# Performance work log

Hardware: AMD Instinct MI355X
Metric: run time of the kernel (lower is better)

## Reference

```python
import jax, jax.numpy as jnp
import numpy as np

N = 20000          # num proposals (nodes)
E = 320000         # num edges
IN = 4096          # roi feature dim
EMB = 200          # glove embed dim
HID = 512          # hidden dim
NH = 8             # heads (conv1)
HC = HID // NH     # 64 per-head channels
NCLS = 151         # VG object classes
NEG_SLOPE = 0.2    # PyG GATConv leaky_relu slope


def setup_inputs() -> dict:
    key = jax.random.key(0)
    ks = jax.random.split(key, 18)
    d_in1 = IN + EMB + 128  # 4424, conv1 input dim
    inp = {
        "roi_features": jax.random.normal(ks[0], (N, IN), jnp.float32),
        "box_info": jax.random.uniform(ks[1], (N, 9), jnp.float32),
        # embedding tables
        "emb1": jax.random.normal(ks[2], (NCLS, EMB), jnp.float32) * 0.02,
        "emb2": jax.random.normal(ks[3], (NCLS, EMB), jnp.float32) * 0.02,
        # bbox MLP 9 -> 32 -> 128
        "bw1": jax.random.normal(ks[4], (9, 32), jnp.float32) / np.sqrt(9),
        "bb1": jnp.zeros((32,), jnp.float32),
        "bw2": jax.random.normal(ks[5], (32, 128), jnp.float32) / np.sqrt(32),
        "bb2": jnp.zeros((128,), jnp.float32),
        # GATConv1: d_in1 -> 8 heads x 64, concat
        "W1": jax.random.normal(ks[6], (d_in1, NH * HC), jnp.float32) / np.sqrt(d_in1),
        "a_src1": jax.random.normal(ks[7], (NH, HC), jnp.float32) * 0.1,
        "a_dst1": jax.random.normal(ks[8], (NH, HC), jnp.float32) * 0.1,
        "bias1": jnp.zeros((NH * HC,), jnp.float32),
        # GATConv2: 512 -> 512, 1 head, concat=False
        "W2": jax.random.normal(ks[9], (HID, HID), jnp.float32) / np.sqrt(HID),
        "a_src2": jax.random.normal(ks[10], (1, HID), jnp.float32) * 0.1,
        "a_dst2": jax.random.normal(ks[11], (1, HID), jnp.float32) * 0.1,
        "bias2": jnp.zeros((HID,), jnp.float32),
        # int inputs
        "obj_labels": jax.random.randint(ks[12], (N,), 0, NCLS, jnp.int32),
        "edge_index": jax.random.randint(ks[13], (2, E), 0, N, jnp.int32),
    }
    return inp


def _segment_softmax(logits, seg, n):
    # logits: [E, H]; softmax over edges sharing the same destination seg id
    m = jax.ops.segment_max(logits, seg, num_segments=n)
    e = jnp.exp(logits - m[seg])
    s = jax.ops.segment_sum(e, seg, num_segments=n)
    return e / (s[seg] + 1e-16)


def _gat_conv(x, src, dst, W, a_src, a_dst, bias, concat):
    # PyG GATConv (self-loops already included in src/dst); dropout off (eval)
    n = x.shape[0]
    H, C = a_src.shape
    h = (x @ W).reshape(n, H, C)                      # [N, H, C]
    al_s = jnp.einsum('nhc,hc->nh', h, a_src)         # [N, H]
    al_d = jnp.einsum('nhc,hc->nh', h, a_dst)
    logits = jax.nn.leaky_relu(al_s[src] + al_d[dst], NEG_SLOPE)  # [E, H]
    alpha = _segment_softmax(logits, dst, n)          # [E, H]
    out = jax.ops.segment_sum(alpha[:, :, None] * h[src], dst, num_segments=n)
    out = out.reshape(n, H * C) if concat else out.mean(axis=1)
    return out + bias


def reference(roi_features, box_info, emb1, emb2, bw1, bb1, bw2, bb2,
              W1, a_src1, a_dst1, bias1, W2, a_src2, a_dst2, bias2,
              obj_labels, edge_index):
    n = roi_features.shape[0]
    # predcls mode: GT labels -> embedding lookup
    obj_embed = emb1[obj_labels]                              # [N, 200]
    pos = jax.nn.relu(box_info @ bw1 + bb1)
    pos = jax.nn.relu(pos @ bw2 + bb2)                        # [N, 128]
    x = jnp.concatenate([roi_features, obj_embed, pos], -1)  # [N, 4424]

    # add self-loops (PyG GATConv default)
    ar = jnp.arange(n, dtype=edge_index.dtype)
    src = jnp.concatenate([edge_index[0], ar])
    dst = jnp.concatenate([edge_index[1], ar])

    edge_f1 = jax.nn.elu(_gat_conv(x, src, dst, W1, a_src1, a_dst1, bias1, True))
    obj_feats = _gat_conv(edge_f1, src, dst, W2, a_src2, a_dst2, bias2, False)

    obj_dists = jax.nn.one_hot(obj_labels, NCLS, dtype=jnp.float32)
    edge_pre_rep = jnp.concatenate([roi_features, obj_feats, emb2[obj_labels]], -1)
    return obj_dists, obj_labels, edge_pre_rep
```

## Files before the change

### kernel.cpp

```cpp
#include <hip/hip_runtime.h>
#include <hip/hip_bf16.h>

#define NNODES 20000
#define NEDGES 320000
#define ETOT   (NEDGES + NNODES)
#define KPADX  4224
#define SK     4
#define KC     (KPADX / SK)
#define MPAD   20096
#define NCLS   151
#define EPRW   4808
#define OUT_LAB_OFF  3020000L
#define OUT_EPR_OFF  3040000L
#define NSLOPE 0.2f

typedef __attribute__((ext_vector_type(8))) short bf16x8;
typedef __attribute__((ext_vector_type(4))) float f32x4;
typedef __attribute__((ext_vector_type(4))) short s16x4;

__device__ __forceinline__ short f2bf(float v) {
  union { __hip_bfloat16 b; short s; } u;
  u.b = __float2bfloat16(v);
  return u.s;
}

__device__ __forceinline__ float bf2f(short s) {
  union { float f; unsigned u; } x;
  x.u = ((unsigned)(unsigned short)s) << 16;
  return x.f;
}

__device__ __forceinline__ void gld16(const short* g, short* l) {
  __builtin_amdgcn_global_load_lds(
      (const __attribute__((address_space(1))) unsigned int*)g,
      (__attribute__((address_space(3))) unsigned int*)l, 16, 0, 0);
}

#define QB0 10000
#define QB1 (QB0 + 5000)
#define QB2 (QB1 + 1584)
#define QB3 (QB2 + 2112)
#define QB4 (QB3 + 256)
#define QB5 (QB4 + 1329)
#define QB6 (QB5 + 151)

__global__ __launch_bounds__(256) void mega_prep_kernel(
    const float* __restrict__ roi, const float* __restrict__ box,
    const float* __restrict__ emb1, const float* __restrict__ emb2,
    const float* __restrict__ bw1, const float* __restrict__ bb1,
    const float* __restrict__ bw2, const float* __restrict__ bb2,
    const float* __restrict__ W1, const float* __restrict__ W2,
    const int* __restrict__ labels, const int* __restrict__ ei,
    short* __restrict__ x, short* __restrict__ w1t, short* __restrict__ w2t,
    short* __restrict__ ef1, int* __restrict__ deg,
    float* __restrict__ als2, float* __restrict__ ald2,
    float* __restrict__ E1, float* __restrict__ dout) {
  const int b = blockIdx.x;
  const int tid = threadIdx.x;

  __shared__ float hids[4][32];
  __shared__ float tile[32][33];

  if (b < QB0) {
    const int base = b * 2048 + tid;
    f32x4 v[8];
#pragma unroll
    for (int k = 0; k < 8; ++k)
      v[k] = *(const f32x4*)&roi[(long)(base + k * 256) * 4];
#pragma unroll
    for (int k = 0; k < 8; ++k) {
      const int t = base + k * 256;
      const int node = t >> 10, cq = t & 1023;
      __builtin_nontemporal_store(v[k],
          (f32x4*)&dout[OUT_EPR_OFF + (long)node * EPRW + cq * 4]);
      s16x4 bb;
      bb.x = f2bf(v[k].x); bb.y = f2bf(v[k].y);
      bb.z = f2bf(v[k].z); bb.w = f2bf(v[k].w);
      *(s16x4*)&x[(long)node * KPADX + cq * 4] = bb;
    }
  } else if (b < QB1) {
    const int w = tid >> 6;
    const int lane = tid & 63;
    const int nd = (b - QB0) * 4 + w;
    if (lane < 32) {
      float a = bb1[lane];
#pragma unroll
      for (int i = 0; i < 9; ++i) a += box[nd * 9 + i] * bw1[i * 32 + lane];
      hids[w][lane] = a > 0.f ? a : 0.f;
    }
    __syncthreads();
    const long xrow = (long)nd * KPADX;
#pragma unroll
    for (int jj = 0; jj < 2; ++jj) {
      const int j = lane + jj * 64;
      float a = bb2[j];
#pragma unroll
      for (int i = 0; i < 32; ++i) a += hids[w][i] * bw2[i * 128 + j];
      a = a > 0.f ? a : 0.f;
      x[xrow + 4096 + j] = f2bf(a);
    }
    const int lab = labels[nd];
    float* epr = dout + OUT_EPR_OFF + (long)nd * EPRW;
    if (lane < 50) {
      const f32x4 e2 = *(const f32x4*)&emb2[lab * 200 + lane * 4];
      __builtin_nontemporal_store(e2, (f32x4*)&epr[4608 + lane * 4]);
    }
    for (int j = lane; j < NCLS; j += 64)
      dout[(long)nd * NCLS + j] = (j == lab) ? 1.f : 0.f;
    if (lane == 0) dout[OUT_LAB_OFF + nd] = (float)lab;
  } else if (b < QB2) {
    const int t = (b - QB1) * 256 + tid;
    if (t < 96 * KPADX) x[(long)NNODES * KPADX + t] = 0;
    if (t < 96 * 512)   ef1[(long)NNODES * 512 + t] = 0;
    if (t < MPAD)       { als2[t] = 0.f; ald2[t] = 0.f; }
  } else if (b < QB3) {
    const int t = b - QB2;
    const int n0 = (t % 16) * 32;
    const int k0 = (t / 16) * 32;
    const int tx = tid & 31, ty = tid >> 5;
#pragma unroll
    for (int i = ty; i < 32; i += 8) {
      const int kp = k0 + i;
      const int src = kp < 4096 ? kp : kp + 200;
      tile[i][tx] = W1[(long)src * 512 + (n0 + tx)];
    }
    __syncthreads();
#pragma unroll
    for (int i = ty; i < 32; i += 8)
      w1t[(long)(n0 + i) * KPADX + (k0 + tx)] = f2bf(tile[tx][i]);
  } else if (b < QB4) {
    const int t = b - QB3;
    const int n0 = (t % 16) * 32;
    const int k0 = (t / 16) * 32;
    const int tx = tid & 31, ty = tid >> 5;
#pragma unroll
    for (int i = ty; i < 32; i += 8)
      tile[i][tx] = W2[(long)(k0 + i) * 512 + (n0 + tx)];
    __syncthreads();
#pragma unroll
    for (int i = ty; i < 32; i += 8)
      w2t[(long)(n0 + i) * 512 + (k0 + tx)] = f2bf(tile[tx][i]);
  } else if (b < QB5) {
    const int e = (b - QB4) * 256 + tid;
    if (e < ETOT) {
      const int d = (e < NEDGES) ? ei[NEDGES + e] : (e - NEDGES);
      atomicAdd(&deg[d], 1);
    }
  } else {
    const int c = b - QB5;
#pragma unroll
    for (int jj = 0; jj < 2; ++jj) {
      const int j = tid + jj * 256;
      float a = 0.f;
      for (int k = 0; k < 200; ++k)
        a += emb1[c * 200 + k] * W1[(long)(4096 + k) * 512 + j];
      E1[c * 512 + j] = a;
    }
  }
}

__global__ __launch_bounds__(256) void scan_kernel(const int* __restrict__ deg,
                                                   int* __restrict__ off,
                                                   int* __restrict__ cur) {
  __shared__ int part[256];
  const int tid = threadIdx.x;
  const int chunk = (NNODES + 255) / 256;
  int start = tid * chunk;
  int end = start + chunk; if (end > NNODES) end = NNODES;
  int s = 0;
  for (int i = start; i < end; ++i) s += deg[i];
  part[tid] = s;
  __syncthreads();
  for (int d = 1; d < 256; d <<= 1) {
    const int v = (tid >= d) ? part[tid - d] : 0;
    __syncthreads();
    part[tid] += v;
    __syncthreads();
  }
  int base = part[tid] - s;
  for (int i = start; i < end; ++i) { off[i] = base; cur[i] = base; base += deg[i]; }
}

__global__ void csr_fill_kernel(const int* __restrict__ ei, int* __restrict__ cur,
                                int* __restrict__ csrs) {
  const int e = blockIdx.x * 256 + threadIdx.x;
  if (e >= ETOT) return;
  const int s = (e < NEDGES) ? ei[e] : (e - NEDGES);
  const int d = (e < NEDGES) ? ei[NEDGES + e] : (e - NEDGES);
  unsigned slot = (unsigned)atomicAdd(&cur[d], 1);
  if (slot >= ETOT) slot = 0;
  csrs[slot] = s;
}

__global__ __launch_bounds__(256) void gemm_split(const short* __restrict__ A,
                                                  const short* __restrict__ BT,
                                                  short* __restrict__ hp) {
  __shared__ short As[4096];
  __shared__ short Bs[4096];
  const int tid = threadIdx.x;
  const int lane = tid & 63;
  const int w = tid >> 6;
  const int wr = w >> 1, wc = w & 1;
  const int wid = (blockIdx.x & 7) * 314 + ((int)blockIdx.x >> 3);
  const long bm = (long)(wid >> 4) * 128;
  const int  sk = (wid >> 2) & 3;
  const long bn = (long)(wid & 3) * 128;

  f32x4 acc[4][4] = {};

  const short* gA0 = A + (bm + w * 32 + (lane >> 2)) * (long)KPADX + sk * KC + (lane & 3) * 8;
  const short* gA1 = gA0 + 16L * KPADX;
  const short* gB0 = BT + (bn + w * 32 + (lane >> 2)) * (long)KPADX + sk * KC + (lane & 3) * 8;
  const short* gB1 = gB0 + 16L * KPADX;
  short* lA0 = &As[w * 1024];
  short* lA1 = &As[w * 1024 + 512];
  short* lB0 = &Bs[w * 1024];
  short* lB1 = &Bs[w * 1024 + 512];

  const int ar = (wr * 64 + (lane & 15)) * 32 + (lane >> 4) * 8;
  const int br = (wc * 64 + (lane & 15)) * 32 + (lane >> 4) * 8;

  for (int k0 = 0; k0 < KC; k0 += 32) {
    gld16(gA0, lA0); gld16(gA1, lA1);
    gld16(gB0, lB0); gld16(gB1, lB1);
    gA0 += 32; gA1 += 32; gB0 += 32; gB1 += 32;
    asm volatile("s_waitcnt vmcnt(0)" ::: "memory");
    __syncthreads();
    bf16x8 a[4], b[4];
#pragma unroll
    for (int mi = 0; mi < 4; ++mi) a[mi] = *(const bf16x8*)&As[ar + mi * 512];
#pragma unroll
    for (int ni = 0; ni < 4; ++ni) b[ni] = *(const bf16x8*)&Bs[br + ni * 512];
#pragma unroll
    for (int mi = 0; mi < 4; ++mi)
#pragma unroll
      for (int ni = 0; ni < 4; ++ni)
        acc[mi][ni] = __builtin_amdgcn_mfma_f32_16x16x32_bf16(a[mi], b[ni], acc[mi][ni], 0, 0, 0);
    __syncthreads();
  }

  short* Cp = hp + (long)sk * MPAD * 512;
#pragma unroll
  for (int mi = 0; mi < 4; ++mi) {
#pragma unroll
    for (int ni = 0; ni < 4; ++ni) {
      const long row0 = bm + wr * 64 + mi * 16 + (lane >> 4) * 4;
      const long col  = bn + wc * 64 + ni * 16 + (lane & 15);
#pragma unroll
      for (int r = 0; r < 4; ++r)
        Cp[(row0 + r) * 512 + col] = f2bf(acc[mi][ni][r]);
    }
  }
}

__global__ __launch_bounds__(256) void reduce1_kernel(short* __restrict__ hp,
    const float* __restrict__ E1, const int* __restrict__ labels,
    const float* __restrict__ aS, const float* __restrict__ aD,
    float* __restrict__ als, float* __restrict__ ald) {
  const int row = blockIdx.x * 4 + (threadIdx.x >> 6);
  const int lane = threadIdx.x & 63;
  const int c0 = lane * 8;
  const long base = (long)row * 512 + c0;
  float v[8] = {};
#pragma unroll
  for (int s = 0; s < SK; ++s) {
    const bf16x8 p = *(const bf16x8*)&hp[(long)s * MPAD * 512 + base];
#pragma unroll
    for (int j = 0; j < 8; ++j) v[j] += bf2f(p[j]);
  }
  const int lab = (row < NNODES) ? labels[row] : 0;
  const float* e1r = E1 + (long)lab * 512;
#pragma unroll
  for (int j = 0; j < 8; ++j) v[j] += e1r[c0 + j];
  bf16x8 o;
#pragma unroll
  for (int j = 0; j < 8; ++j) o[j] = f2bf(v[j]);
  *(bf16x8*)&hp[base] = o;
  float s_ = 0.f, d_ = 0.f;
#pragma unroll
  for (int j = 0; j < 8; ++j) {
    s_ += v[j] * aS[c0 + j];
    d_ += v[j] * aD[c0 + j];
  }
#pragma unroll
  for (int oo = 1; oo < 8; oo <<= 1) {
    s_ += __shfl_xor(s_, oo);
    d_ += __shfl_xor(d_, oo);
  }
  if ((lane & 7) == 0) {
    const int head = lane >> 3;
    als[row * 8 + head] = s_;
    ald[row * 8 + head] = d_;
  }
}

__global__ __launch_bounds__(256) void gemm_bt(const short* __restrict__ A,
                                               const short* __restrict__ BT,
                                               short* __restrict__ C,
                                               const float* __restrict__ aS,
                                               const float* __restrict__ aD,
                                               float* __restrict__ als,
                                               float* __restrict__ ald,
                                               int Kpad, int Ncols, int H) {
  __shared__ short As[4096];
  __shared__ short Bs[4096];
  const int tid = threadIdx.x;
  const int lane = tid & 63;
  const int w = tid >> 6;
  const int wr = w >> 1, wc = w & 1;
  const int nbn = Ncols >> 7;
  const long bm = (long)((int)blockIdx.x / nbn) * 128;
  const long bn = (long)((int)blockIdx.x % nbn) * 128;

  f32x4 acc[4][4] = {};

  const short* gA0 = A + (bm + w * 32 + (lane >> 2)) * (long)Kpad + (lane & 3) * 8;
  const short* gA1 = gA0 + 16L * Kpad;
  const short* gB0 = BT + (bn + w * 32 + (lane >> 2)) * (long)Kpad + (lane & 3) * 8;
  const short* gB1 = gB0 + 16L * Kpad;
  short* lA0 = &As[w * 1024];
  short* lA1 = &As[w * 1024 + 512];
  short* lB0 = &Bs[w * 1024];
  short* lB1 = &Bs[w * 1024 + 512];

  const int ar = (wr * 64 + (lane & 15)) * 32 + (lane >> 4) * 8;
  const int br = (wc * 64 + (lane & 15)) * 32 + (lane >> 4) * 8;

  for (int k0 = 0; k0 < Kpad; k0 += 32) {
    gld16(gA0, lA0); gld16(gA1, lA1);
    gld16(gB0, lB0); gld16(gB1, lB1);
    gA0 += 32; gA1 += 32; gB0 += 32; gB1 += 32;
    asm volatile("s_waitcnt vmcnt(0)" ::: "memory");
    __syncthreads();
    bf16x8 a[4], b[4];
#pragma unroll
    for (int mi = 0; mi < 4; ++mi) a[mi] = *(const bf16x8*)&As[ar + mi * 512];
#pragma unroll
    for (int ni = 0; ni < 4; ++ni) b[ni] = *(const bf16x8*)&Bs[br + ni * 512];
#pragma unroll
    for (int mi = 0; mi < 4; ++mi)
#pragma unroll
      for (int ni = 0; ni < 4; ++ni)
        acc[mi][ni] = __builtin_amdgcn_mfma_f32_16x16x32_bf16(a[mi], b[ni], acc[mi][ni], 0, 0, 0);
    __syncthreads();
  }

  const int colb = (int)bn + wc * 64 + (lane & 15);

#pragma unroll
  for (int mi = 0; mi < 4; ++mi) {
#pragma unroll
    for (int ni = 0; ni < 4; ++ni) {
      const long row0 = bm + wr * 64 + mi * 16 + (lane >> 4) * 4;
      const long col  = bn + wc * 64 + ni * 16 + (lane & 15);
#pragma unroll
      for (int r = 0; r < 4; ++r)
        C[(row0 + r) * (long)Ncols + col] = f2bf(acc[mi][ni][r]);
    }
  }

  float asv[4], adv[4];
#pragma unroll
  for (int ni = 0; ni < 4; ++ni) {
    asv[ni] = aS[colb + ni * 16];
    adv[ni] = aD[colb + ni * 16];
  }
  const int head = (H == 8) ? (((int)bn >> 6) + wc) : 0;
#pragma unroll
  for (int mi = 0; mi < 4; ++mi) {
#pragma unroll
    for (int r = 0; r < 4; ++r) {
      float s = 0.f, d = 0.f;
#pragma unroll
      for (int ni = 0; ni < 4; ++ni) {
        const float v = acc[mi][ni][r];
        s += v * asv[ni];
        d += v * adv[ni];
      }
#pragma unroll
      for (int o = 1; o < 16; o <<= 1) {
        s += __shfl_xor(s, o);
        d += __shfl_xor(d, o);
      }
      if ((lane & 15) == 0) {
        const long row = bm + wr * 64 + mi * 16 + (lane >> 4) * 4 + r;
        atomicAdd(&als[row * H + head], s);
        atomicAdd(&ald[row * H + head], d);
      }
    }
  }
}

__global__ __launch_bounds__(256) void gather1_kernel(const int* __restrict__ off,
    const int* __restrict__ csrs,
    const float* __restrict__ als, const float* __restrict__ ald,
    const short* __restrict__ h1, const float* __restrict__ bias,
    short* __restrict__ ef1) {
  const int dn = blockIdx.x * 4 + (threadIdx.x >> 6);
  const int lane = threadIdx.x & 63;
  const int c0 = lane * 8;
  const int head = lane >> 3;
  const int beg = off[dn];
  const int end = (dn == NNODES - 1) ? ETOT : off[dn + 1];
  const float ad = ald[dn * 8 + head];
  float sum = 0.f;
  float acc[8] = {};
  for (int i = beg; i < end; ++i) {
    int s = csrs[i];
    if ((unsigned)s >= NNODES) s = 0;
    float l = als[s * 8 + head] + ad;
    l = l > 0.f ? l : NSLOPE * l;
    const float wgt = expf(l);
    sum += wgt;
    const bf16x8 hv = *(const bf16x8*)&h1[(long)s * 512 + c0];
#pragma unroll
    for (int j = 0; j < 8; ++j) acc[j] += wgt * bf2f(hv[j]);
  }
  const float inv = 1.f / (sum + 1e-16f);
  bf16x8 outv;
#pragma unroll
  for (int j = 0; j < 8; ++j) {
    float r = acc[j] * inv + bias[c0 + j];
    r = r > 0.f ? r : expm1f(r);
    outv[j] = f2bf(r);
  }
  *(bf16x8*)&ef1[(long)dn * 512 + c0] = outv;
}

__global__ __launch_bounds__(256) void gather2_kernel(const int* __restrict__ off,
    const int* __restrict__ csrs,
    const float* __restrict__ als, const float* __restrict__ ald,
    const short* __restrict__ h2, const float* __restrict__ bias,
    float* __restrict__ dout) {
  const int dn = blockIdx.x * 4 + (threadIdx.x >> 6);
  const int lane = threadIdx.x & 63;
  const int c0 = lane * 8;
  const int beg = off[dn];
  const int end = (dn == NNODES - 1) ? ETOT : off[dn + 1];
  const float ad = ald[dn];
  float sum = 0.f;
  float acc[8] = {};
  for (int i = beg; i < end; ++i) {
    int s = csrs[i];
    if ((unsigned)s >= NNODES) s = 0;
    float l = als[s] + ad;
    l = l > 0.f ? l : NSLOPE * l;
    const float wgt = expf(l);
    sum += wgt;
    const bf16x8 hv = *(const bf16x8*)&h2[(long)s * 512 + c0];
#pragma unroll
    for (int j = 0; j < 8; ++j) acc[j] += wgt * bf2f(hv[j]);
  }
  const float inv = 1.f / (sum + 1e-16f);
  float* epr = dout + OUT_EPR_OFF + (long)dn * EPRW + 4096;
  f32x4 o0, o1;
  o0.x = acc[0] * inv + bias[c0 + 0];
  o0.y = acc[1] * inv + bias[c0 + 1];
  o0.z = acc[2] * inv + bias[c0 + 2];
  o0.w = acc[3] * inv + bias[c0 + 3];
  o1.x = acc[4] * inv + bias[c0 + 4];
  o1.y = acc[5] * inv + bias[c0 + 5];
  o1.z = acc[6] * inv + bias[c0 + 6];
  o1.w = acc[7] * inv + bias[c0 + 7];
  __builtin_nontemporal_store(o0, (f32x4*)&epr[c0]);
  __builtin_nontemporal_store(o1, (f32x4*)&epr[c0 + 4]);
}

extern "C" void kernel_launch(void* const* d_in, const int* in_sizes, int n_in,
                              void* d_out, int out_size, void* d_ws, size_t ws_size,
                              hipStream_t stream) {
  const float* roi  = (const float*)d_in[0];
  const float* box  = (const float*)d_in[1];
  const float* emb1 = (const float*)d_in[2];
  const float* emb2 = (const float*)d_in[3];
  const float* bw1  = (const float*)d_in[4];
  const float* bb1  = (const float*)d_in[5];
  const float* bw2  = (const float*)d_in[6];
  const float* bb2  = (const float*)d_in[7];
  const float* W1   = (const float*)d_in[8];
  const float* as1  = (const float*)d_in[9];
  const float* ad1  = (const float*)d_in[10];
  const float* b1   = (const float*)d_in[11];
  const float* W2   = (const float*)d_in[12];
  const float* as2  = (const float*)d_in[13];
  const float* ad2  = (const float*)d_in[14];
  const float* b2   = (const float*)d_in[15];
  const int* labels = (const int*)d_in[16];
  const int* ei     = (const int*)d_in[17];
  float* dout = (float*)d_out;

  char* wsb = (char*)d_ws;
  size_t o = 0;
  auto alloc = [&](size_t bytes) -> void* {
    void* p = wsb + o;
    o += (bytes + 255) & ~(size_t)255;
    return p;
  };
  short* x    = (short*)alloc((size_t)MPAD * KPADX * 2);
  short* w1t  = (short*)alloc((size_t)512 * KPADX * 2);
  short* hp   = (short*)alloc((size_t)SK * MPAD * 512 * 2);
  short* h1   = hp;
  short* ef1  = (short*)alloc((size_t)MPAD * 512 * 2);
  short* w2t  = (short*)alloc((size_t)512 * 512 * 2);
  short* h2   = (short*)alloc((size_t)MPAD * 512 * 2);
  float* als1 = (float*)alloc((size_t)MPAD * 8 * 4);
  float* ald1 = (float*)alloc((size_t)MPAD * 8 * 4);
  float* als2 = (float*)alloc((size_t)MPAD * 4);
  float* ald2 = (float*)alloc((size_t)MPAD * 4);
  float* E1   = (float*)alloc((size_t)NCLS * 512 * 4);
  int*   deg  = (int*)alloc((size_t)NNODES * 4);
  int*   offs = (int*)alloc((size_t)NNODES * 4);
  int*   cur  = (int*)alloc((size_t)NNODES * 4);
  int*   csrs = (int*)alloc((size_t)ETOT * 4);

  const int EB = (ETOT + 255) / 256;

  hipMemsetAsync(deg, 0, (size_t)NNODES * 4, stream);

  hipLaunchKernelGGL(mega_prep_kernel, dim3(QB6), dim3(256), 0, stream,
                     roi, box, emb1, emb2, bw1, bb1, bw2, bb2, W1, W2,
                     labels, ei, x, w1t, w2t, ef1, deg,
                     als2, ald2, E1, dout);
  hipLaunchKernelGGL(scan_kernel, dim3(1), dim3(256), 0, stream, deg, offs, cur);
  hipLaunchKernelGGL(csr_fill_kernel, dim3(EB), dim3(256), 0, stream, ei, cur, csrs);
  hipLaunchKernelGGL(gemm_split, dim3(157 * SK * 4), dim3(256), 0, stream,
                     x, w1t, hp);
  hipLaunchKernelGGL(reduce1_kernel, dim3(MPAD / 4), dim3(256), 0, stream,
                     hp, E1, labels, as1, ad1, als1, ald1);
  hipLaunchKernelGGL(gather1_kernel, dim3(NNODES / 4), dim3(256), 0, stream,
                     offs, csrs, als1, ald1, h1, b1, ef1);
  hipLaunchKernelGGL(gemm_bt, dim3(157 * 4), dim3(256), 0, stream,
                     ef1, w2t, h2, as2, ad2, als2, ald2, 512, 512, 1);
  hipLaunchKernelGGL(gather2_kernel, dim3(NNODES / 4), dim3(256), 0, stream,
                     offs, csrs, als2, ald2, h2, b2, dout);
}
```

Baseline: 558.2 us.

## Move fp32 roi copy into GEMM launch to overlap with matmul

The prep kernel now only converts roi features to bf16, using 8-wide loads and nontemporal 16-byte stores with half as many blocks. The fp32 copy of roi into the edge_pre_rep output moves into extra trailing blocks of the split-K GEMM launch. The aim is to hide that memory-bound copy behind the compute-bound GEMM. The risk is that the copy blocks compete with the GEMM for bandwidth and cache, and the GEMM must wait for its own extra blocks before the launch finishes.

```diff
diff --git a/kernel.cpp b/kernel.cpp
--- a/kernel.cpp
+++ b/kernel.cpp
@@ -13,6 +13,8 @@
 #define OUT_LAB_OFF  3020000L
 #define OUT_EPR_OFF  3040000L
 #define NSLOPE 0.2f
+#define NGEMM1 2512
+#define NCOPY  10000
 
 typedef __attribute__((ext_vector_type(8))) short bf16x8;
 typedef __attribute__((ext_vector_type(4))) float f32x4;
@@ -36,7 +38,7 @@
       (__attribute__((address_space(3))) unsigned int*)l, 16, 0, 0);
 }
 
-#define QB0 10000
+#define QB0 5000
 #define QB1 (QB0 + 5000)
 #define QB2 (QB1 + 1584)
 #define QB3 (QB2 + 2112)
@@ -62,21 +64,25 @@
   __shared__ float tile[32][33];
 
   if (b < QB0) {
-    const int base = b * 2048 + tid;
-    f32x4 v[8];
-#pragma unroll
-    for (int k = 0; k < 8; ++k)
-      v[k] = *(const f32x4*)&roi[(long)(base + k * 256) * 4];
+    const int c0 = b * 2048 + tid;
+    f32x4 v0[8], v1[8];
 #pragma unroll
     for (int k = 0; k < 8; ++k) {
-      const int t = base + k * 256;
-      const int node = t >> 10, cq = t & 1023;
-      __builtin_nontemporal_store(v[k],
-          (f32x4*)&dout[OUT_EPR_OFF + (long)node * EPRW + cq * 4]);
-      s16x4 bb;
-      bb.x = f2bf(v[k].x); bb.y = f2bf(v[k].y);
-      bb.z = f2bf(v[k].z); bb.w = f2bf(v[k].w);
-      *(s16x4*)&x[(long)node * KPADX + cq * 4] = bb;
+      const int c = c0 + k * 256;
+      const float* src = &roi[((long)(c >> 9) << 12) + (c & 511) * 8];
+      v0[k] = *(const f32x4*)src;
+      v1[k] = *(const f32x4*)(src + 4);
+    }
+#pragma unroll
+    for (int k = 0; k < 8; ++k) {
+      const int c = c0 + k * 256;
+      bf16x8 bb;
+      bb[0] = f2bf(v0[k].x); bb[1] = f2bf(v0[k].y);
+      bb[2] = f2bf(v0[k].z); bb[3] = f2bf(v0[k].w);
+      bb[4] = f2bf(v1[k].x); bb[5] = f2bf(v1[k].y);
+      bb[6] = f2bf(v1[k].z); bb[7] = f2bf(v1[k].w);
+      __builtin_nontemporal_store(bb,
+          (bf16x8*)&x[(long)(c >> 9) * KPADX + (c & 511) * 8]);
     }
   } else if (b < QB1) {
     const int w = tid >> 6;
@@ -194,10 +200,29 @@
 
 __global__ __launch_bounds__(256) void gemm_split(const short* __restrict__ A,
                                                   const short* __restrict__ BT,
-                                                  short* __restrict__ hp) {
+                                                  short* __restrict__ hp,
+                                                  const float* __restrict__ roi,
+                                                  float* __restrict__ dout) {
+  const int tid = threadIdx.x;
+  if ((int)blockIdx.x >= NGEMM1) {
+    const int t = (int)blockIdx.x - NGEMM1;
+    const int c0 = t * 2048 + tid;
+    f32x4 v[8];
+#pragma unroll
+    for (int k = 0; k < 8; ++k) {
+      const int c = c0 + k * 256;
+      v[k] = *(const f32x4*)&roi[((long)(c >> 10) << 12) + (c & 1023) * 4];
+    }
+#pragma unroll
+    for (int k = 0; k < 8; ++k) {
+      const int c = c0 + k * 256;
+      __builtin_nontemporal_store(v[k],
+          (f32x4*)&dout[OUT_EPR_OFF + (long)(c >> 10) * EPRW + (c & 1023) * 4]);
+    }
+    return;
+  }
   __shared__ short As[4096];
   __shared__ short Bs[4096];
-  const int tid = threadIdx.x;
   const int lane = tid & 63;
   const int w = tid >> 6;
   const int wr = w >> 1, wc = w & 1;
@@ -523,8 +548,8 @@
                      als2, ald2, E1, dout);
   hipLaunchKernelGGL(scan_kernel, dim3(1), dim3(256), 0, stream, deg, offs, cur);
   hipLaunchKernelGGL(csr_fill_kernel, dim3(EB), dim3(256), 0, stream, ei, cur, csrs);
-  hipLaunchKernelGGL(gemm_split, dim3(157 * SK * 4), dim3(256), 0, stream,
-                     x, w1t, hp);
+  hipLaunchKernelGGL(gemm_split, dim3(NGEMM1 + NCOPY), dim3(256), 0, stream,
+                     x, w1t, hp, roi, dout);
   hipLaunchKernelGGL(reduce1_kernel, dim3(MPAD / 4), dim3(256), 0, stream,
                      hp, E1, labels, as1, ad1, als1, ald1);
   hipLaunchKernelGGL(gather1_kernel, dim3(NNODES / 4), dim3(256), 0, stream,
```

New measurement: 606.3 us. +8.6%, slower.
